# Optimization experiments

Measured on AMD Instinct MI355X. Metric: run time of the kernel, lower is better.

## Reference

```python
import jax, jax.numpy as jnp
import numpy as np

N = 100000      # nodes
E = 1000000     # edges
G = 1024        # graphs
NODE_IN, CLIMBER_IN, HID, OUT, HEADS = 6, 4, 64, 4, 2
SLOPE = 0.2     # PyG GATConv default negative_slope


def gat_conv(x, edge_index, W, att_src, att_dst, bias):
    """PyG GATConv, heads=HEADS, concat=False (mean over heads), add_self_loops=True."""
    heads, ch = att_src.shape
    xp = (x @ W).reshape(-1, heads, ch)                       # [N,H,C]
    a_src = jnp.einsum('nhc,hc->nh', xp, att_src)             # [N,H]
    a_dst = jnp.einsum('nhc,hc->nh', xp, att_dst)
    loops = jnp.arange(x.shape[0])
    src = jnp.concatenate([edge_index[0], loops])             # [E+N]
    dst = jnp.concatenate([edge_index[1], loops])
    e = jax.nn.leaky_relu(a_src[src] + a_dst[dst], SLOPE)     # [E+N,H]
    emax = jax.ops.segment_max(e, dst, num_segments=x.shape[0])
    emax = jnp.where(jnp.isfinite(emax), emax, 0.0)
    ex = jnp.exp(e - emax[dst])
    den = jax.ops.segment_sum(ex, dst, num_segments=x.shape[0])
    alpha = ex / (den[dst] + 1e-16)                           # segment softmax over incoming edges
    msg = xp[src] * alpha[:, :, None]                         # [E+N,H,C]
    agg = jax.ops.segment_sum(msg, dst, num_segments=x.shape[0])  # [N,H,C]
    return agg.mean(axis=1) + bias                            # concat=False -> head mean


def setup_inputs() -> dict:
    key = jax.random.key(0)
    ks = jax.random.split(key, 20)
    s = lambda *d: 1.0 / np.sqrt(d[0])
    inp = {
        'x': jax.random.normal(ks[0], (N, NODE_IN), jnp.float32),
        'edge_index': jax.random.randint(ks[1], (2, E), 0, N),
        'batch': jnp.sort(jax.random.randint(ks[2], (N,), 0, G)),
        'climber': jax.random.normal(ks[3], (G, CLIMBER_IN), jnp.float32),
        # conv1 params
        'W1': jax.random.normal(ks[4], (NODE_IN, HEADS * HID), jnp.float32) * s(NODE_IN),
        'as1': jax.random.normal(ks[5], (HEADS, HID), jnp.float32) * s(HID),
        'ad1': jax.random.normal(ks[6], (HEADS, HID), jnp.float32) * s(HID),
        'b1': jnp.zeros((HID,), jnp.float32),
        # conv2 params
        'W2': jax.random.normal(ks[7], (HID, HEADS * HID), jnp.float32) * s(HID),
        'as2': jax.random.normal(ks[8], (HEADS, HID), jnp.float32) * s(HID),
        'ad2': jax.random.normal(ks[9], (HEADS, HID), jnp.float32) * s(HID),
        'b2': jnp.zeros((HID,), jnp.float32),
        # climber embed
        'Wc': jax.random.normal(ks[10], (CLIMBER_IN, HID), jnp.float32) * s(CLIMBER_IN),
        'bc': jnp.zeros((HID,), jnp.float32),
        # classifier
        'Wm1': jax.random.normal(ks[11], (2 * HID, HID), jnp.float32) * s(2 * HID),
        'bm1': jnp.zeros((HID,), jnp.float32),
        'Wm2': jax.random.normal(ks[12], (HID, OUT), jnp.float32) * s(HID),
        'bm2': jnp.zeros((OUT,), jnp.float32),
    }
    return inp


def reference(x, edge_index, batch, climber, W1, as1, ad1, b1, W2, as2, ad2, b2,
              Wc, bc, Wm1, bm1, Wm2, bm2):
    h = jax.nn.relu(gat_conv(x, edge_index, W1, as1, ad1, b1))
    h = jax.nn.relu(gat_conv(h, edge_index, W2, as2, ad2, b2))
    c = jax.nn.relu(climber @ Wc + bc)            # dropout is identity in eval mode
    z = jnp.concatenate([h, c[batch]], axis=1)    # [N, 2*HID]
    z = jax.nn.relu(z @ Wm1 + bm1)                # dropout identity (eval)
    return z @ Wm2 + bm2                          # [N, OUT]
```

## Files before the change

kernel.cpp:

```cpp
#include <hip/hip_runtime.h>
#include <hip/hip_fp16.h>

#define SLOPE 0.2f
#define BKW  512
#define BKSH 9
#define MAXB 256

__device__ __forceinline__ float lrelu(float v) { return v >= 0.f ? v : SLOPE * v; }

__device__ __forceinline__ unsigned pack2(float a, float b) {
    __half2 h = __floats2half2_rn(a, b);
    return *reinterpret_cast<unsigned*>(&h);
}
__device__ __forceinline__ float2 h2f(unsigned u) {
    __half2 h = *reinterpret_cast<__half2*>(&u);
    return __half22float2(h);
}

__device__ __forceinline__ void pk8(unsigned& A0, unsigned& A1, unsigned& A2, unsigned& A3,
                                    unsigned ap, uint4 u) {
    __half2 a = *reinterpret_cast<__half2*>(&ap);
    __half2* up = reinterpret_cast<__half2*>(&u);
    *reinterpret_cast<__half2*>(&A0) = __hfma2(up[0], a, *reinterpret_cast<__half2*>(&A0));
    *reinterpret_cast<__half2*>(&A1) = __hfma2(up[1], a, *reinterpret_cast<__half2*>(&A1));
    *reinterpret_cast<__half2*>(&A2) = __hfma2(up[2], a, *reinterpret_cast<__half2*>(&A2));
    *reinterpret_cast<__half2*>(&A3) = __hfma2(up[3], a, *reinterpret_cast<__half2*>(&A3));
}

__global__ __launch_bounds__(256)
void k_xp_gemm64h(const __half* __restrict__ x, const float* __restrict__ W,
                  const float* __restrict__ as_, const float* __restrict__ ad_,
                  __half* __restrict__ xph, float* __restrict__ asrc,
                  float* __restrict__ adst, int N) {
    constexpr int K = 64;
    constexpr int ZS = K + 1;
    __shared__ float zs[64 * ZS];
    __shared__ float ws[K * 128];
    const int n0 = blockIdx.x * 64;
    const int t = threadIdx.x;

    for (int i = t; i < K * 32; i += 256) ((float4*)ws)[i] = ((const float4*)W)[i];
    for (int i = t; i < 64 * 8; i += 256) {
        int n = i >> 3, k8 = i & 7;
        int gn = n0 + n;
        uint4 v = make_uint4(0u, 0u, 0u, 0u);
        if (gn < N) v = ((const uint4*)x)[(size_t)gn * 8 + k8];
        float2 f0 = h2f(v.x), f1 = h2f(v.y), f2 = h2f(v.z), f3 = h2f(v.w);
        float* zr = zs + n * ZS + k8 * 8;
        zr[0] = f0.x; zr[1] = f0.y; zr[2] = f1.x; zr[3] = f1.y;
        zr[4] = f2.x; zr[5] = f2.y; zr[6] = f3.x; zr[7] = f3.y;
    }
    __syncthreads();

    const int tx = t & 15, ty = t >> 4;
    const int c0a = tx * 4;
    const int c0b = 64 + tx * 4;

    float4 asA = *(const float4*)(as_ + c0a);
    float4 asB = *(const float4*)(as_ + c0b);
    float4 adA = *(const float4*)(ad_ + c0a);
    float4 adB = *(const float4*)(ad_ + c0b);

    float acc[4][8];
    #pragma unroll
    for (int i = 0; i < 4; ++i)
        #pragma unroll
        for (int j = 0; j < 8; ++j) acc[i][j] = 0.f;

    for (int k = 0; k < K; ++k) {
        float4 w0 = *(const float4*)(ws + k * 128 + c0a);
        float4 w1 = *(const float4*)(ws + k * 128 + c0b);
        #pragma unroll
        for (int i = 0; i < 4; ++i) {
            float zv = zs[(ty * 4 + i) * ZS + k];
            acc[i][0] += zv * w0.x; acc[i][1] += zv * w0.y;
            acc[i][2] += zv * w0.z; acc[i][3] += zv * w0.w;
            acc[i][4] += zv * w1.x; acc[i][5] += zv * w1.y;
            acc[i][6] += zv * w1.z; acc[i][7] += zv * w1.w;
        }
    }

    #pragma unroll
    for (int i = 0; i < 4; ++i) {
        int nl = ty * 4 + i, gn = n0 + nl;
        if (gn < N) {
            uint2 ua, ub;
            ua.x = pack2(acc[i][0], acc[i][1]);
            ua.y = pack2(acc[i][2], acc[i][3]);
            ub.x = pack2(acc[i][4], acc[i][5]);
            ub.y = pack2(acc[i][6], acc[i][7]);
            *(uint2*)(xph + (size_t)gn * 128 + c0a) = ua;
            *(uint2*)(xph + (size_t)gn * 128 + c0b) = ub;
        }
        float ps0 = acc[i][0]*asA.x + acc[i][1]*asA.y + acc[i][2]*asA.z + acc[i][3]*asA.w;
        float ps1 = acc[i][4]*asB.x + acc[i][5]*asB.y + acc[i][6]*asB.z + acc[i][7]*asB.w;
        float pd0 = acc[i][0]*adA.x + acc[i][1]*adA.y + acc[i][2]*adA.z + acc[i][3]*adA.w;
        float pd1 = acc[i][4]*adB.x + acc[i][5]*adB.y + acc[i][6]*adB.z + acc[i][7]*adB.w;
        #pragma unroll
        for (int off = 1; off <= 8; off <<= 1) {
            ps0 += __shfl_xor(ps0, off, 64);
            ps1 += __shfl_xor(ps1, off, 64);
            pd0 += __shfl_xor(pd0, off, 64);
            pd1 += __shfl_xor(pd1, off, 64);
        }
        if (tx == 0 && gn < N) {
            asrc[gn * 2]     = ps0;
            asrc[gn * 2 + 1] = ps1;
            adst[gn * 2]     = pd0;
            adst[gn * 2 + 1] = pd1;
        }
    }
}

__global__ __launch_bounds__(256)
void k_bcount(const int* __restrict__ dst, int* __restrict__ bkt_cnt, int E, int nb) {
    __shared__ int cnt[MAXB];
    int t = threadIdx.x;
    for (int i = t; i < MAXB; i += 256) cnt[i] = 0;
    __syncthreads();
    int be = blockIdx.x * 4096;
    int n = min(4096, E - be);
    const int4* d4 = (const int4*)(dst + be);
    #pragma unroll
    for (int i = 0; i < 4; ++i) {
        int j = t + 256 * i, r = j * 4;
        if (r < n) {
            int4 d = d4[j];
            if (r + 0 < n) atomicAdd(&cnt[d.x >> BKSH], 1);
            if (r + 1 < n) atomicAdd(&cnt[d.y >> BKSH], 1);
            if (r + 2 < n) atomicAdd(&cnt[d.z >> BKSH], 1);
            if (r + 3 < n) atomicAdd(&cnt[d.w >> BKSH], 1);
        }
    }
    __syncthreads();
    for (int b = t; b < nb; b += 256) if (cnt[b]) atomicAdd(&bkt_cnt[b], cnt[b]);
}

__global__ __launch_bounds__(256)
void k_bscan(const int* __restrict__ bkt_cnt, int* __restrict__ bkt_base,
             int* __restrict__ bkt_cur, int nb, int E) {
    __shared__ int sh[256];
    int t = threadIdx.x;
    int v = (t < nb) ? bkt_cnt[t] : 0;
    int orig = v;
    sh[t] = v; __syncthreads();
    for (int off = 1; off < 256; off <<= 1) {
        int u = (t >= off) ? sh[t - off] : 0;
        __syncthreads(); sh[t] += u; __syncthreads();
    }
    int base = sh[t] - orig;
    if (t < nb) { bkt_base[t] = base; bkt_cur[t] = base; }
    if (t == 0) bkt_base[nb] = E;
}

__global__ __launch_bounds__(256)
void k_part(const int* __restrict__ src, const int* __restrict__ dst,
            int* __restrict__ bkt_cur, uint2* __restrict__ ebuf, int E) {
    __shared__ int cnt[MAXB];
    __shared__ int shift[MAXB];
    __shared__ int cur[MAXB];
    __shared__ int sh[256];
    __shared__ uint2 data[4096];
    __shared__ unsigned char bof[4096];
    int t = threadIdx.x;
    cnt[t] = 0;
    __syncthreads();
    int be = blockIdx.x * 4096;
    int n = min(4096, E - be);
    const int4* d4 = (const int4*)(dst + be);
    const int4* s4 = (const int4*)(src + be);
    #pragma unroll
    for (int i = 0; i < 4; ++i) {
        int j = t + 256 * i, r = j * 4;
        if (r < n) {
            int4 d = d4[j];
            if (r + 0 < n) atomicAdd(&cnt[d.x >> BKSH], 1);
            if (r + 1 < n) atomicAdd(&cnt[d.y >> BKSH], 1);
            if (r + 2 < n) atomicAdd(&cnt[d.z >> BKSH], 1);
            if (r + 3 < n) atomicAdd(&cnt[d.w >> BKSH], 1);
        }
    }
    __syncthreads();
    int v = cnt[t], orig = v;
    sh[t] = v; __syncthreads();
    for (int off = 1; off < 256; off <<= 1) {
        int u = (t >= off) ? sh[t - off] : 0;
        __syncthreads(); sh[t] += u; __syncthreads();
    }
    int lb = sh[t] - orig;
    cur[t] = lb;
    if (orig > 0) {
        int g = atomicAdd(&bkt_cur[t], orig);
        shift[t] = g - lb;
    }
    __syncthreads();
    #pragma unroll
    for (int i = 0; i < 4; ++i) {
        int j = t + 256 * i, r = j * 4;
        if (r < n) {
            int4 d = d4[j]; int4 s = s4[j];
            if (r + 0 < n) { int b = d.x >> BKSH; int p = atomicAdd(&cur[b], 1); data[p] = make_uint2((unsigned)s.x, (unsigned)d.x); bof[p] = (unsigned char)b; }
            if (r + 1 < n) { int b = d.y >> BKSH; int p = atomicAdd(&cur[b], 1); data[p] = make_uint2((unsigned)s.y, (unsigned)d.y); bof[p] = (unsigned char)b; }
            if (r + 2 < n) { int b = d.z >> BKSH; int p = atomicAdd(&cur[b], 1); data[p] = make_uint2((unsigned)s.z, (unsigned)d.z); bof[p] = (unsigned char)b; }
            if (r + 3 < n) { int b = d.w >> BKSH; int p = atomicAdd(&cur[b], 1); data[p] = make_uint2((unsigned)s.w, (unsigned)d.w); bof[p] = (unsigned char)b; }
        }
    }
    __syncthreads();
    for (int j = t; j < n; j += 256) {
        int b = bof[j];
        ebuf[shift[b] + j] = data[j];
    }
}

__global__ __launch_bounds__(256)
void k_build(const uint2* __restrict__ ebuf, const int* __restrict__ bkt_base,
             int* __restrict__ rowptr, int* __restrict__ csr_src, int N, int E, int nb,
             const float* __restrict__ x, const float* __restrict__ W1,
             const float* __restrict__ as1, const float* __restrict__ ad1,
             __half* __restrict__ xph, float* __restrict__ asrc,
             float* __restrict__ adst,
             const float* __restrict__ climber, const float* __restrict__ Wc,
             const float* __restrict__ bc, const float* __restrict__ Wm1,
             const float* __restrict__ bm1, float* __restrict__ cpre, int G,
             int nTile) {
    __shared__ char smem[17408];
    __shared__ int sh[256];
    int bid = blockIdx.x;
    const int t = threadIdx.x;

    if (bid < nb) {
        int* deg = (int*)smem;
        int* pre = deg + 512;
        int* cur = pre + 512;
        int n0 = bid << BKSH;
        int nn = min(BKW, N - n0);
        int eb = bkt_base[bid], ee = bkt_base[bid + 1];
        for (int i = t; i < BKW; i += 256) deg[i] = 0;
        __syncthreads();
        for (int j = eb + t; j < ee; j += 256)
            atomicAdd(&deg[(int)ebuf[j].y - n0], 1);
        __syncthreads();
        int a = deg[2 * t], b2 = deg[2 * t + 1];
        int s = a + b2, orig = s;
        sh[t] = s; __syncthreads();
        for (int off = 1; off < 256; off <<= 1) {
            int u = (t >= off) ? sh[t - off] : 0;
            __syncthreads(); sh[t] += u; __syncthreads();
        }
        int base = sh[t] - orig;
        pre[2 * t] = base; pre[2 * t + 1] = base + a;
        cur[2 * t] = base; cur[2 * t + 1] = base + a;
        __syncthreads();
        for (int i = t; i < nn; i += 256) rowptr[n0 + i] = eb + pre[i];
        for (int j = eb + t; j < ee; j += 256) {
            uint2 e = ebuf[j];
            int lp = atomicAdd(&cur[(int)e.y - n0], 1);
            csr_src[eb + lp] = (int)e.x;
        }
        if (bid == 0 && t == 0) rowptr[N] = E;
        return;
    }
    bid -= nb;
    if (bid < nTile) {
        constexpr int K = 6, ZS = 7;
        float* smf = (float*)smem;
        float* zs = smf;
        float* ws = smf + 448;
        const int n0 = bid * 64;

        for (int i = t; i < K * 32; i += 256) ((float4*)ws)[i] = ((const float4*)W1)[i];
        for (int i = t; i < 64 * K; i += 256) {
            int n = i / K, k = i - n * K;
            int gn = n0 + n;
            zs[n * ZS + k] = (gn < N) ? x[(size_t)gn * K + k] : 0.f;
        }
        __syncthreads();

        const int tx = t & 15, ty = t >> 4;
        const int c0a = tx * 4;
        const int c0b = 64 + tx * 4;

        float4 asA = *(const float4*)(as1 + c0a);
        float4 asB = *(const float4*)(as1 + c0b);
        float4 adA = *(const float4*)(ad1 + c0a);
        float4 adB = *(const float4*)(ad1 + c0b);

        float acc[4][8];
        #pragma unroll
        for (int i = 0; i < 4; ++i)
            #pragma unroll
            for (int j = 0; j < 8; ++j) acc[i][j] = 0.f;

        for (int k = 0; k < K; ++k) {
            float4 w0 = *(const float4*)(ws + k * 128 + c0a);
            float4 w1 = *(const float4*)(ws + k * 128 + c0b);
            #pragma unroll
            for (int i = 0; i < 4; ++i) {
                float zv = zs[(ty * 4 + i) * ZS + k];
                acc[i][0] += zv * w0.x; acc[i][1] += zv * w0.y;
                acc[i][2] += zv * w0.z; acc[i][3] += zv * w0.w;
                acc[i][4] += zv * w1.x; acc[i][5] += zv * w1.y;
                acc[i][6] += zv * w1.z; acc[i][7] += zv * w1.w;
            }
        }

        #pragma unroll
        for (int i = 0; i < 4; ++i) {
            int nl = ty * 4 + i, gn = n0 + nl;
            if (gn < N) {
                uint2 ua, ub;
                ua.x = pack2(acc[i][0], acc[i][1]);
                ua.y = pack2(acc[i][2], acc[i][3]);
                ub.x = pack2(acc[i][4], acc[i][5]);
                ub.y = pack2(acc[i][6], acc[i][7]);
                *(uint2*)(xph + (size_t)gn * 128 + c0a) = ua;
                *(uint2*)(xph + (size_t)gn * 128 + c0b) = ub;
            }
            float ps0 = acc[i][0]*asA.x + acc[i][1]*asA.y + acc[i][2]*asA.z + acc[i][3]*asA.w;
            float ps1 = acc[i][4]*asB.x + acc[i][5]*asB.y + acc[i][6]*asB.z + acc[i][7]*asB.w;
            float pd0 = acc[i][0]*adA.x + acc[i][1]*adA.y + acc[i][2]*adA.z + acc[i][3]*adA.w;
            float pd1 = acc[i][4]*adB.x + acc[i][5]*adB.y + acc[i][6]*adB.z + acc[i][7]*adB.w;
            #pragma unroll
            for (int off = 1; off <= 8; off <<= 1) {
                ps0 += __shfl_xor(ps0, off, 64);
                ps1 += __shfl_xor(ps1, off, 64);
                pd0 += __shfl_xor(pd0, off, 64);
                pd1 += __shfl_xor(pd1, off, 64);
            }
            if (tx == 0 && gn < N) {
                asrc[gn * 2]     = ps0;
                asrc[gn * 2 + 1] = ps1;
                adst[gn * 2]     = pd0;
                adst[gn * 2 + 1] = pd1;
            }
        }
        return;
    }
    bid -= nTile;
    {
        float* smf = (float*)smem;
        float* ce   = smf;
        float* wm1b = smf + 256;
        for (int i = t; i < 1024; i += 256) ((float4*)wm1b)[i] = ((const float4*)Wm1)[1024 + i];
        int gl = t >> 6, c = t & 63;
        int g = bid * 4 + gl;
        float acc = bc[c];
        if (g < G)
            for (int k = 0; k < 4; ++k) acc += climber[g * 4 + k] * Wc[k * 64 + c];
        ce[gl * 64 + c] = fmaxf(acc, 0.f);
        __syncthreads();
        float o = bm1[c];
        for (int k = 0; k < 64; ++k) o += ce[gl * 64 + k] * wm1b[k * 64 + c];
        if (g < G) cpre[(size_t)g * 64 + c] = o;
    }
}

__global__ void k_ag(const int* __restrict__ rowptr, const int* __restrict__ csr_src,
                     const float* __restrict__ asrc, const float* __restrict__ adst,
                     const __half* __restrict__ xph, const float* __restrict__ b,
                     __half* __restrict__ hout, int N) {
    int tid = blockIdx.x * blockDim.x + threadIdx.x;
    int lane = threadIdx.x & 63;
    int wid = tid >> 6;
    int nw = (gridDim.x * blockDim.x) >> 6;
    const int l  = lane & 31;
    const int hh = lane >> 5;
    const int g4 = (lane >> 3) & 3;
    const int c8 = lane & 7;
    const int lofs = hh * 8 + c8;
    const uint4* xp4 = (const uint4*)xph;
    float4 bb0 = ((const float4*)b)[c8 * 2];
    float4 bb1 = ((const float4*)b)[c8 * 2 + 1];

    for (int n = wid; n < N; n += nw) {
        int rs = rowptr[n], re = rowptr[n + 1], cnt = re - rs;
        uint4 uself = xp4[(size_t)n * 16 + lofs];
        float a_dst = adst[n * 2 + hh];
        float eself = __expf(lrelu(asrc[n * 2 + hh] + a_dst));

        unsigned A0 = 0u, A1 = 0u, A2 = 0u, A3 = 0u;
        float den;

        if (cnt <= 32) {
            float ev = 0.f; int s_reg = n;
            if (l < cnt) {
                s_reg = csr_src[rs + l];
                ev = __expf(lrelu(asrc[s_reg * 2 + hh] + a_dst));
            }
            unsigned evp = pack2(ev, ev);
            if (g4 == 0) pk8(A0, A1, A2, A3, pack2(eself, eself), uself);

            const int base = (hh << 5) - rs;
            int e0 = rs;
            for (; e0 + 4 < re; e0 += 8) {
                int ea = e0 + g4, eb = e0 + 4 + g4;
                unsigned aa = __shfl(evp,   base + ea, 64);
                int      sa = __shfl(s_reg, base + ea, 64);
                unsigned ab = __shfl(evp,   base + eb, 64);
                int      sb = __shfl(s_reg, base + eb, 64);
                if (eb >= re) { ab = 0u; sb = n; }
                uint4 u1 = xp4[(size_t)sa * 16 + lofs];
                uint4 u2 = xp4[(size_t)sb * 16 + lofs];
                pk8(A0, A1, A2, A3, aa, u1);
                pk8(A0, A1, A2, A3, ab, u2);
            }
            if (e0 < re) {
                int ea = e0 + g4;
                unsigned aa = __shfl(evp,   base + ea, 64);
                int      sa = __shfl(s_reg, base + ea, 64);
                if (ea >= re) { aa = 0u; sa = n; }
                uint4 u1 = xp4[(size_t)sa * 16 + lofs];
                pk8(A0, A1, A2, A3, aa, u1);
            }
            den = ev + (l == 0 ? eself : 0.f);
            #pragma unroll
            for (int off = 16; off > 0; off >>= 1) den += __shfl_xor(den, off, 64);
        } else {
            den = (l == 0) ? eself : 0.f;
            for (int e = rs + l; e < re; e += 32)
                den += __expf(lrelu(asrc[csr_src[e] * 2 + hh] + a_dst));
            #pragma unroll
            for (int off = 16; off > 0; off >>= 1) den += __shfl_xor(den, off, 64);
            if (g4 == 0) pk8(A0, A1, A2, A3, pack2(eself, eself), uself);
            for (int e0 = rs; e0 < re; e0 += 8) {
                int ea = e0 + g4, eb = e0 + 4 + g4;
                bool va = ea < re, vb = eb < re;
                int sa = va ? csr_src[ea] : n;
                int sb = vb ? csr_src[eb] : n;
                float fa = va ? __expf(lrelu(asrc[sa * 2 + hh] + a_dst)) : 0.f;
                float fb = vb ? __expf(lrelu(asrc[sb * 2 + hh] + a_dst)) : 0.f;
                unsigned aa = pack2(fa, fa);
                unsigned ab = pack2(fb, fb);
                uint4 u1 = xp4[(size_t)sa * 16 + lofs];
                uint4 u2 = xp4[(size_t)sb * 16 + lofs];
                pk8(A0, A1, A2, A3, aa, u1);
                pk8(A0, A1, A2, A3, ab, u2);
            }
        }

        float inv = 1.f / (den + 1e-16f);

        float2 f0 = h2f(A0), f1 = h2f(A1), f2 = h2f(A2), f3 = h2f(A3);
        float4 accA = make_float4(f0.x, f0.y, f1.x, f1.y);
        float4 accB = make_float4(f2.x, f2.y, f3.x, f3.y);

        #pragma unroll
        for (int off = 8; off <= 16; off <<= 1) {
            accA.x += __shfl_xor(accA.x, off, 64);
            accA.y += __shfl_xor(accA.y, off, 64);
            accA.z += __shfl_xor(accA.z, off, 64);
            accA.w += __shfl_xor(accA.w, off, 64);
            accB.x += __shfl_xor(accB.x, off, 64);
            accB.y += __shfl_xor(accB.y, off, 64);
            accB.z += __shfl_xor(accB.z, off, 64);
            accB.w += __shfl_xor(accB.w, off, 64);
        }
        accA.x *= inv; accA.y *= inv; accA.z *= inv; accA.w *= inv;
        accB.x *= inv; accB.y *= inv; accB.z *= inv; accB.w *= inv;
        accA.x += __shfl_xor(accA.x, 32, 64);
        accA.y += __shfl_xor(accA.y, 32, 64);
        accA.z += __shfl_xor(accA.z, 32, 64);
        accA.w += __shfl_xor(accA.w, 32, 64);
        accB.x += __shfl_xor(accB.x, 32, 64);
        accB.y += __shfl_xor(accB.y, 32, 64);
        accB.z += __shfl_xor(accB.z, 32, 64);
        accB.w += __shfl_xor(accB.w, 32, 64);

        if (lane < 8) {
            uint4 up;
            up.x = pack2(fmaxf(accA.x * 0.5f + bb0.x, 0.f),
                         fmaxf(accA.y * 0.5f + bb0.y, 0.f));
            up.y = pack2(fmaxf(accA.z * 0.5f + bb0.z, 0.f),
                         fmaxf(accA.w * 0.5f + bb0.w, 0.f));
            up.z = pack2(fmaxf(accB.x * 0.5f + bb1.x, 0.f),
                         fmaxf(accB.y * 0.5f + bb1.y, 0.f));
            up.w = pack2(fmaxf(accB.z * 0.5f + bb1.z, 0.f),
                         fmaxf(accB.w * 0.5f + bb1.w, 0.f));
            ((uint4*)hout)[(size_t)n * 8 + c8] = up;
        }
    }
}

__global__ __launch_bounds__(256)
void k_final(const __half* __restrict__ h2, const float* __restrict__ cpre,
             const int* __restrict__ batch, const float* __restrict__ Wm1,
             const float* __restrict__ Wm2, const float* __restrict__ bm2,
             float* __restrict__ out, int N) {
    __shared__ float zs[64 * 65];
    __shared__ float ws[64 * 64];
    __shared__ float4 w2l[64];
    const int n0 = blockIdx.x * 64;
    const int t = threadIdx.x;

    for (int i = t; i < 1024; i += 256) ((float4*)ws)[i] = ((const float4*)Wm1)[i];
    if (t < 64) w2l[t] = ((const float4*)Wm2)[t];
    for (int i = t; i < 64 * 8; i += 256) {
        int n = i >> 3, k8 = i & 7;
        int gn = n0 + n;
        uint4 v = make_uint4(0u, 0u, 0u, 0u);
        if (gn < N) v = ((const uint4*)h2)[(size_t)gn * 8 + k8];
        float2 f0 = h2f(v.x), f1 = h2f(v.y), f2 = h2f(v.z), f3 = h2f(v.w);
        float* zr = zs + n * 65 + k8 * 8;
        zr[0] = f0.x; zr[1] = f0.y; zr[2] = f1.x; zr[3] = f1.y;
        zr[4] = f2.x; zr[5] = f2.y; zr[6] = f3.x; zr[7] = f3.y;
    }
    __syncthreads();

    const int tx = t & 15, ty = t >> 4;
    const int c0 = tx * 4;
    float acc[4][4];
    #pragma unroll
    for (int i = 0; i < 4; ++i)
        #pragma unroll
        for (int j = 0; j < 4; ++j) acc[i][j] = 0.f;

    for (int k = 0; k < 64; ++k) {
        float4 wv = *(const float4*)(ws + k * 64 + c0);
        #pragma unroll
        for (int i = 0; i < 4; ++i) {
            float zv = zs[(ty * 4 + i) * 65 + k];
            acc[i][0] += zv * wv.x; acc[i][1] += zv * wv.y;
            acc[i][2] += zv * wv.z; acc[i][3] += zv * wv.w;
        }
    }
    __syncthreads();

    float4 wa = w2l[c0], wb = w2l[c0 + 1], wc = w2l[c0 + 2], wd = w2l[c0 + 3];
    #pragma unroll
    for (int i = 0; i < 4; ++i) {
        int nl = ty * 4 + i, gn = n0 + nl;
        float4 o = make_float4(0.f, 0.f, 0.f, 0.f);
        if (gn < N) {
            int b = batch[gn];
            float4 cp = *(const float4*)(cpre + (size_t)b * 64 + c0);
            float m0 = fmaxf(acc[i][0] + cp.x, 0.f);
            float m1 = fmaxf(acc[i][1] + cp.y, 0.f);
            float m2 = fmaxf(acc[i][2] + cp.z, 0.f);
            float m3 = fmaxf(acc[i][3] + cp.w, 0.f);
            o.x = m0 * wa.x + m1 * wb.x + m2 * wc.x + m3 * wd.x;
            o.y = m0 * wa.y + m1 * wb.y + m2 * wc.y + m3 * wd.y;
            o.z = m0 * wa.z + m1 * wb.z + m2 * wc.z + m3 * wd.z;
            o.w = m0 * wa.w + m1 * wb.w + m2 * wc.w + m3 * wd.w;
        }
        *(float4*)(zs + tx * 260 + nl * 4) = o;
    }
    __syncthreads();
    {
        int nl = t >> 2, j = t & 3, gn = n0 + nl;
        float s = 0.f;
        #pragma unroll
        for (int tx2 = 0; tx2 < 16; ++tx2) s += zs[tx2 * 260 + nl * 4 + j];
        if (gn < N) out[(size_t)gn * 4 + j] = s + bm2[j];
    }
}

extern "C" void kernel_launch(void* const* d_in, const int* in_sizes, int n_in,
                              void* d_out, int out_size, void* d_ws, size_t ws_size,
                              hipStream_t stream) {
    const float* x       = (const float*)d_in[0];
    const int*   ei      = (const int*)  d_in[1];
    const int*   batch   = (const int*)  d_in[2];
    const float* climber = (const float*)d_in[3];
    const float* W1  = (const float*)d_in[4];
    const float* as1 = (const float*)d_in[5];
    const float* ad1 = (const float*)d_in[6];
    const float* b1  = (const float*)d_in[7];
    const float* W2  = (const float*)d_in[8];
    const float* as2 = (const float*)d_in[9];
    const float* ad2 = (const float*)d_in[10];
    const float* b2  = (const float*)d_in[11];
    const float* Wc  = (const float*)d_in[12];
    const float* bc  = (const float*)d_in[13];
    const float* Wm1 = (const float*)d_in[14];
    const float* bm1 = (const float*)d_in[15];
    const float* Wm2 = (const float*)d_in[16];
    const float* bm2 = (const float*)d_in[17];

    const int N  = in_sizes[0] / 6;
    const int E  = in_sizes[1] / 2;
    const int G  = in_sizes[3] / 4;

    const int* srcI = ei;
    const int* dstI = ei + E;

    char* base = (char*)d_ws;
    size_t off = 0;
    auto carve = [&](size_t bytes) { void* p = base + off; off += (bytes + 255) & ~size_t(255); return p; };
    __half* xph    = (__half*)carve((size_t)N * 128 * 2);
    __half* hbuf   = (__half*)carve((size_t)N * 64 * 2);
    float* asrc    = (float*)carve((size_t)N * 2 * 4);
    float* adst    = (float*)carve((size_t)N * 2 * 4);
    float* cpre    = (float*)carve((size_t)G * 64 * 4);
    int*   rowptr  = (int*)  carve((size_t)(N + 1) * 4);
    int*   csr_src = (int*)  carve((size_t)E * 4);
    uint2* ebuf    = (uint2*)carve((size_t)E * 8);
    int*   bkt_cnt = (int*)  carve((size_t)MAXB * 4);
    int*   bkt_base= (int*)  carve((size_t)(MAXB + 1) * 4);
    int*   bkt_cur = (int*)  carve((size_t)MAXB * 4);

    const int tpb = 256;
    const int nb = (N + BKW - 1) >> BKSH;
    const int nChunk = (E + 4095) / 4096;
    const int nClimber = (G + 3) / 4;
    const int PG = 2048;
    const int nTile = (N + 63) / 64;

    hipMemsetAsync(bkt_cnt, 0, (size_t)nb * 4, stream);
    k_bcount<<<nChunk, tpb, 0, stream>>>(dstI, bkt_cnt, E, nb);
    k_bscan<<<1, tpb, 0, stream>>>(bkt_cnt, bkt_base, bkt_cur, nb, E);
    k_part<<<nChunk, tpb, 0, stream>>>(srcI, dstI, bkt_cur, ebuf, E);
    k_build<<<nb + nTile + nClimber, tpb, 0, stream>>>(
        ebuf, bkt_base, rowptr, csr_src, N, E, nb,
        x, W1, as1, ad1, xph, asrc, adst,
        climber, Wc, bc, Wm1, bm1, cpre, G, nTile);

    k_ag<<<PG, tpb, 0, stream>>>(rowptr, csr_src, asrc, adst, xph, b1, hbuf, N);

    k_xp_gemm64h<<<nTile, tpb, 0, stream>>>(hbuf, W2, as2, ad2, xph, asrc, adst, N);
    k_ag<<<PG, tpb, 0, stream>>>(rowptr, csr_src, asrc, adst, xph, b2, hbuf, N);

    k_final<<<nTile, tpb, 0, stream>>>(hbuf, cpre, batch, Wm1, Wm2, bm2, (float*)d_out, N);
}
```

Measured before the change: 281.0 us.

## Use MFMA fp16 for second-layer projection and pack edge buffer to 32-bit

The second GAT projection GEMM now uses 16x16x32 fp16 MFMA instructions with a pre-transposed fp16 copy of W2, built in a spare block of the scan kernel. Results are staged through LDS so each row is written to global memory as coalesced vectors. Separately, the partitioned edge buffer packs the source index and the local destination offset into one 32-bit word instead of a uint2, halving that traffic. The risks are reduced precision from fp16 weights and a reliance on source indices fitting in 23 bits.

```diff
diff --git a/kernel.cpp b/kernel.cpp
--- a/kernel.cpp
+++ b/kernel.cpp
@@ -5,6 +5,9 @@
 #define BKW  512
 #define BKSH 9
 #define MAXB 256
+
+typedef _Float16 half8 __attribute__((ext_vector_type(8)));
+typedef float f32x4 __attribute__((ext_vector_type(4)));
 
 __device__ __forceinline__ float lrelu(float v) { return v >= 0.f ? v : SLOPE * v; }
 
@@ -28,86 +31,93 @@
 }
 
 __global__ __launch_bounds__(256)
-void k_xp_gemm64h(const __half* __restrict__ x, const float* __restrict__ W,
+void k_xp_gemm64h(const __half* __restrict__ x, const _Float16* __restrict__ W2t,
                   const float* __restrict__ as_, const float* __restrict__ ad_,
                   __half* __restrict__ xph, float* __restrict__ asrc,
                   float* __restrict__ adst, int N) {
-    constexpr int K = 64;
-    constexpr int ZS = K + 1;
-    __shared__ float zs[64 * ZS];
-    __shared__ float ws[K * 128];
-    const int n0 = blockIdx.x * 64;
+    __shared__ __half lh[4][16][128];
     const int t = threadIdx.x;
-
-    for (int i = t; i < K * 32; i += 256) ((float4*)ws)[i] = ((const float4*)W)[i];
-    for (int i = t; i < 64 * 8; i += 256) {
-        int n = i >> 3, k8 = i & 7;
-        int gn = n0 + n;
-        uint4 v = make_uint4(0u, 0u, 0u, 0u);
-        if (gn < N) v = ((const uint4*)x)[(size_t)gn * 8 + k8];
-        float2 f0 = h2f(v.x), f1 = h2f(v.y), f2 = h2f(v.z), f3 = h2f(v.w);
-        float* zr = zs + n * ZS + k8 * 8;
-        zr[0] = f0.x; zr[1] = f0.y; zr[2] = f1.x; zr[3] = f1.y;
-        zr[4] = f2.x; zr[5] = f2.y; zr[6] = f3.x; zr[7] = f3.y;
-    }
-    __syncthreads();
-
-    const int tx = t & 15, ty = t >> 4;
-    const int c0a = tx * 4;
-    const int c0b = 64 + tx * 4;
-
-    float4 asA = *(const float4*)(as_ + c0a);
-    float4 asB = *(const float4*)(as_ + c0b);
-    float4 adA = *(const float4*)(ad_ + c0a);
-    float4 adB = *(const float4*)(ad_ + c0b);
-
-    float acc[4][8];
-    #pragma unroll
-    for (int i = 0; i < 4; ++i)
-        #pragma unroll
-        for (int j = 0; j < 8; ++j) acc[i][j] = 0.f;
-
-    for (int k = 0; k < K; ++k) {
-        float4 w0 = *(const float4*)(ws + k * 128 + c0a);
-        float4 w1 = *(const float4*)(ws + k * 128 + c0b);
-        #pragma unroll
-        for (int i = 0; i < 4; ++i) {
-            float zv = zs[(ty * 4 + i) * ZS + k];
-            acc[i][0] += zv * w0.x; acc[i][1] += zv * w0.y;
-            acc[i][2] += zv * w0.z; acc[i][3] += zv * w0.w;
-            acc[i][4] += zv * w1.x; acc[i][5] += zv * w1.y;
-            acc[i][6] += zv * w1.z; acc[i][7] += zv * w1.w;
-        }
-    }
-
-    #pragma unroll
-    for (int i = 0; i < 4; ++i) {
-        int nl = ty * 4 + i, gn = n0 + nl;
+    const int w = t >> 6, lane = t & 63;
+    const int c8 = lane & 15, kgrp = lane >> 4;
+    const int nr0 = blockIdx.x * 64 + w * 16;
+
+    uint4 a0u = make_uint4(0u,0u,0u,0u), a1u = make_uint4(0u,0u,0u,0u);
+    int ar = nr0 + c8;
+    if (ar < N) {
+        const uint4* hp = (const uint4*)(x + (size_t)ar * 64);
+        a0u = hp[kgrp];
+        a1u = hp[4 + kgrp];
+    }
+    half8 A0, A1;
+    __builtin_memcpy(&A0, &a0u, 16);
+    __builtin_memcpy(&A1, &a1u, 16);
+
+    f32x4 acc[8];
+    #pragma unroll
+    for (int i = 0; i < 8; ++i) acc[i] = (f32x4){0.f, 0.f, 0.f, 0.f};
+
+    #pragma unroll
+    for (int ct = 0; ct < 8; ++ct) {
+        const uint4* wp = (const uint4*)(W2t + (size_t)(ct * 16 + c8) * 64);
+        uint4 b0u = wp[kgrp];
+        uint4 b1u = wp[4 + kgrp];
+        half8 B0, B1;
+        __builtin_memcpy(&B0, &b0u, 16);
+        __builtin_memcpy(&B1, &b1u, 16);
+        acc[ct] = __builtin_amdgcn_mfma_f32_16x16x32_f16(A0, B0, acc[ct], 0, 0, 0);
+        acc[ct] = __builtin_amdgcn_mfma_f32_16x16x32_f16(A1, B1, acc[ct], 0, 0, 0);
+    }
+
+    float ps0[4] = {0,0,0,0}, ps1[4] = {0,0,0,0};
+    float pd0[4] = {0,0,0,0}, pd1[4] = {0,0,0,0};
+    #pragma unroll
+    for (int ct = 0; ct < 8; ++ct) {
+        float av = as_[ct * 16 + c8];
+        float dv = ad_[ct * 16 + c8];
+        #pragma unroll
+        for (int j = 0; j < 4; ++j) {
+            float v = acc[ct][j];
+            if (ct < 4) { ps0[j] += av * v; pd0[j] += dv * v; }
+            else        { ps1[j] += av * v; pd1[j] += dv * v; }
+        }
+    }
+    #pragma unroll
+    for (int off = 1; off <= 8; off <<= 1) {
+        #pragma unroll
+        for (int j = 0; j < 4; ++j) {
+            ps0[j] += __shfl_xor(ps0[j], off, 64);
+            ps1[j] += __shfl_xor(ps1[j], off, 64);
+            pd0[j] += __shfl_xor(pd0[j], off, 64);
+            pd1[j] += __shfl_xor(pd1[j], off, 64);
+        }
+    }
+    if (c8 == 0) {
+        #pragma unroll
+        for (int j = 0; j < 4; ++j) {
+            int gn = nr0 + kgrp * 4 + j;
+            if (gn < N) {
+                asrc[gn * 2]     = ps0[j];
+                asrc[gn * 2 + 1] = ps1[j];
+                adst[gn * 2]     = pd0[j];
+                adst[gn * 2 + 1] = pd1[j];
+            }
+        }
+    }
+
+    #pragma unroll
+    for (int ct = 0; ct < 8; ++ct)
+        #pragma unroll
+        for (int j = 0; j < 4; ++j)
+            lh[w][kgrp * 4 + j][ct * 16 + c8] = __float2half(acc[ct][j]);
+    __syncthreads();
+    {
+        int r = lane >> 2, q = lane & 3;
+        int gn = nr0 + r;
         if (gn < N) {
-            uint2 ua, ub;
-            ua.x = pack2(acc[i][0], acc[i][1]);
-            ua.y = pack2(acc[i][2], acc[i][3]);
-            ub.x = pack2(acc[i][4], acc[i][5]);
-            ub.y = pack2(acc[i][6], acc[i][7]);
-            *(uint2*)(xph + (size_t)gn * 128 + c0a) = ua;
-            *(uint2*)(xph + (size_t)gn * 128 + c0b) = ub;
-        }
-        float ps0 = acc[i][0]*asA.x + acc[i][1]*asA.y + acc[i][2]*asA.z + acc[i][3]*asA.w;
-        float ps1 = acc[i][4]*asB.x + acc[i][5]*asB.y + acc[i][6]*asB.z + acc[i][7]*asB.w;
-        float pd0 = acc[i][0]*adA.x + acc[i][1]*adA.y + acc[i][2]*adA.z + acc[i][3]*adA.w;
-        float pd1 = acc[i][4]*adB.x + acc[i][5]*adB.y + acc[i][6]*adB.z + acc[i][7]*adB.w;
-        #pragma unroll
-        for (int off = 1; off <= 8; off <<= 1) {
-            ps0 += __shfl_xor(ps0, off, 64);
-            ps1 += __shfl_xor(ps1, off, 64);
-            pd0 += __shfl_xor(pd0, off, 64);
-            pd1 += __shfl_xor(pd1, off, 64);
-        }
-        if (tx == 0 && gn < N) {
-            asrc[gn * 2]     = ps0;
-            asrc[gn * 2 + 1] = ps1;
-            adst[gn * 2]     = pd0;
-            adst[gn * 2 + 1] = pd1;
+            const uint4* srow = (const uint4*)&lh[w][r][0];
+            uint4* drow = (uint4*)(xph + (size_t)gn * 128);
+            #pragma unroll
+            for (int c4 = 0; c4 < 4; ++c4) drow[q * 4 + c4] = srow[q * 4 + c4];
         }
     }
 }
@@ -137,10 +147,18 @@
 }
 
 __global__ __launch_bounds__(256)
-void k_bscan(const int* __restrict__ bkt_cnt, int* __restrict__ bkt_base,
-             int* __restrict__ bkt_cur, int nb, int E) {
+void k_bscan_prep(const int* __restrict__ bkt_cnt, int* __restrict__ bkt_base,
+                  int* __restrict__ bkt_cur, int nb, int E,
+                  const float* __restrict__ W2, _Float16* __restrict__ W2t) {
+    int t = threadIdx.x;
+    if (blockIdx.x == 1) {
+        for (int i = t; i < 128 * 64; i += 256) {
+            int c = i >> 6, k = i & 63;
+            W2t[i] = (_Float16)W2[k * 128 + c];
+        }
+        return;
+    }
     __shared__ int sh[256];
-    int t = threadIdx.x;
     int v = (t < nb) ? bkt_cnt[t] : 0;
     int orig = v;
     sh[t] = v; __syncthreads();
@@ -155,12 +173,12 @@
 
 __global__ __launch_bounds__(256)
 void k_part(const int* __restrict__ src, const int* __restrict__ dst,
-            int* __restrict__ bkt_cur, uint2* __restrict__ ebuf, int E) {
+            int* __restrict__ bkt_cur, unsigned* __restrict__ ebuf, int E) {
     __shared__ int cnt[MAXB];
     __shared__ int shift[MAXB];
     __shared__ int cur[MAXB];
     __shared__ int sh[256];
-    __shared__ uint2 data[4096];
+    __shared__ unsigned data[4096];
     __shared__ unsigned char bof[4096];
     int t = threadIdx.x;
     cnt[t] = 0;
@@ -199,10 +217,10 @@
         int j = t + 256 * i, r = j * 4;
         if (r < n) {
             int4 d = d4[j]; int4 s = s4[j];
-            if (r + 0 < n) { int b = d.x >> BKSH; int p = atomicAdd(&cur[b], 1); data[p] = make_uint2((unsigned)s.x, (unsigned)d.x); bof[p] = (unsigned char)b; }
-            if (r + 1 < n) { int b = d.y >> BKSH; int p = atomicAdd(&cur[b], 1); data[p] = make_uint2((unsigned)s.y, (unsigned)d.y); bof[p] = (unsigned char)b; }
-            if (r + 2 < n) { int b = d.z >> BKSH; int p = atomicAdd(&cur[b], 1); data[p] = make_uint2((unsigned)s.z, (unsigned)d.z); bof[p] = (unsigned char)b; }
-            if (r + 3 < n) { int b = d.w >> BKSH; int p = atomicAdd(&cur[b], 1); data[p] = make_uint2((unsigned)s.w, (unsigned)d.w); bof[p] = (unsigned char)b; }
+            if (r + 0 < n) { int b = d.x >> BKSH; int p = atomicAdd(&cur[b], 1); data[p] = ((unsigned)s.x << BKSH) | (unsigned)(d.x & (BKW-1)); bof[p] = (unsigned char)b; }
+            if (r + 1 < n) { int b = d.y >> BKSH; int p = atomicAdd(&cur[b], 1); data[p] = ((unsigned)s.y << BKSH) | (unsigned)(d.y & (BKW-1)); bof[p] = (unsigned char)b; }
+            if (r + 2 < n) { int b = d.z >> BKSH; int p = atomicAdd(&cur[b], 1); data[p] = ((unsigned)s.z << BKSH) | (unsigned)(d.z & (BKW-1)); bof[p] = (unsigned char)b; }
+            if (r + 3 < n) { int b = d.w >> BKSH; int p = atomicAdd(&cur[b], 1); data[p] = ((unsigned)s.w << BKSH) | (unsigned)(d.w & (BKW-1)); bof[p] = (unsigned char)b; }
         }
     }
     __syncthreads();
@@ -213,7 +231,7 @@
 }
 
 __global__ __launch_bounds__(256)
-void k_build(const uint2* __restrict__ ebuf, const int* __restrict__ bkt_base,
+void k_build(const unsigned* __restrict__ ebuf, const int* __restrict__ bkt_base,
              int* __restrict__ rowptr, int* __restrict__ csr_src, int N, int E, int nb,
              const float* __restrict__ x, const float* __restrict__ W1,
              const float* __restrict__ as1, const float* __restrict__ ad1,
@@ -238,7 +256,7 @@
         for (int i = t; i < BKW; i += 256) deg[i] = 0;
         __syncthreads();
         for (int j = eb + t; j < ee; j += 256)
-            atomicAdd(&deg[(int)ebuf[j].y - n0], 1);
+            atomicAdd(&deg[ebuf[j] & (BKW - 1)], 1);
         __syncthreads();
         int a = deg[2 * t], b2 = deg[2 * t + 1];
         int s = a + b2, orig = s;
@@ -253,9 +271,9 @@
         __syncthreads();
         for (int i = t; i < nn; i += 256) rowptr[n0 + i] = eb + pre[i];
         for (int j = eb + t; j < ee; j += 256) {
-            uint2 e = ebuf[j];
-            int lp = atomicAdd(&cur[(int)e.y - n0], 1);
-            csr_src[eb + lp] = (int)e.x;
+            unsigned e = ebuf[j];
+            int lp = atomicAdd(&cur[e & (BKW - 1)], 1);
+            csr_src[eb + lp] = (int)(e >> BKSH);
         }
         if (bid == 0 && t == 0) rowptr[N] = E;
         return;
@@ -593,10 +611,11 @@
     float* cpre    = (float*)carve((size_t)G * 64 * 4);
     int*   rowptr  = (int*)  carve((size_t)(N + 1) * 4);
     int*   csr_src = (int*)  carve((size_t)E * 4);
-    uint2* ebuf    = (uint2*)carve((size_t)E * 8);
+    unsigned* ebuf = (unsigned*)carve((size_t)E * 4);
     int*   bkt_cnt = (int*)  carve((size_t)MAXB * 4);
     int*   bkt_base= (int*)  carve((size_t)(MAXB + 1) * 4);
     int*   bkt_cur = (int*)  carve((size_t)MAXB * 4);
+    _Float16* W2t  = (_Float16*)carve((size_t)128 * 64 * 2);
 
     const int tpb = 256;
     const int nb = (N + BKW - 1) >> BKSH;
@@ -607,7 +626,7 @@
 
     hipMemsetAsync(bkt_cnt, 0, (size_t)nb * 4, stream);
     k_bcount<<<nChunk, tpb, 0, stream>>>(dstI, bkt_cnt, E, nb);
-    k_bscan<<<1, tpb, 0, stream>>>(bkt_cnt, bkt_base, bkt_cur, nb, E);
+    k_bscan_prep<<<2, tpb, 0, stream>>>(bkt_cnt, bkt_base, bkt_cur, nb, E, W2, W2t);
     k_part<<<nChunk, tpb, 0, stream>>>(srcI, dstI, bkt_cur, ebuf, E);
     k_build<<<nb + nTile + nClimber, tpb, 0, stream>>>(
         ebuf, bkt_base, rowptr, csr_src, N, E, nb,
@@ -616,7 +635,7 @@
 
     k_ag<<<PG, tpb, 0, stream>>>(rowptr, csr_src, asrc, adst, xph, b1, hbuf, N);
 
-    k_xp_gemm64h<<<nTile, tpb, 0, stream>>>(hbuf, W2, as2, ad2, xph, asrc, adst, N);
+    k_xp_gemm64h<<<nTile, tpb, 0, stream>>>(hbuf, W2t, as2, ad2, xph, asrc, adst, N);
     k_ag<<<PG, tpb, 0, stream>>>(rowptr, csr_src, asrc, adst, xph, b2, hbuf, N);
 
     k_final<<<nTile, tpb, 0, stream>>>(hbuf, cpre, batch, Wm1, Wm2, bm2, (float*)d_out, N);
```

After: 276.6 us (median of 2 runs). No clear change (-1.6%).
